# Kernel optimization log

Measured on AMD Instinct MI355X. Metric: run time of the kernel, lower is better.

The kernel has to match this reference:

```python
import jax, jax.numpy as jnp
import numpy as np

HARDSHRINK_LAMBDA = 0.75

def setup_inputs() -> dict:
    key = jax.random.key(0)
    k1, k2, k3, k4, k5 = jax.random.split(key, 5)
    B, Cin, H, W = 32, 3, 128, 128
    Cmid, Dout = 256, 4096
    x = jax.random.normal(k1, (B, Cin, H, W), dtype=jnp.float32)
    # Conv2d(3,256,k=3,p=1) params, kaiming-ish scale
    conv_w = jax.random.normal(k2, (Cmid, Cin, 3, 3), dtype=jnp.float32) * (1.0 / np.sqrt(Cin * 9))
    conv_b = jax.random.normal(k3, (Cmid,), dtype=jnp.float32) * 0.01
    fc_w = jax.random.normal(k4, (Dout, Cmid), dtype=jnp.float32) * (1.0 / np.sqrt(Cmid))
    fc_b = jax.random.normal(k5, (Dout,), dtype=jnp.float32) * 0.01
    return {"x": x, "conv_w": conv_w, "conv_b": conv_b, "fc_w": fc_w, "fc_b": fc_b}

def reference(x, conv_w, conv_b, fc_w, fc_b):
    # Conv2d stride=1, padding=1  -> [B, Cmid, H, W]
    y = jax.lax.conv_general_dilated(
        x, conv_w, window_strides=(1, 1), padding=((1, 1), (1, 1)),
        dimension_numbers=("NCHW", "OIHW", "NCHW"))
    y = y + conv_b[None, :, None, None]
    y = jax.nn.relu(y)
    # Nearest upsample (integer scale) replicates each value s*s times; the
    # subsequent elementwise hardshrink then global average pool is therefore
    y = jnp.where(jnp.abs(y) > HARDSHRINK_LAMBDA, y, 0.0)
    pooled = jnp.mean(y, axis=(2, 3))  # [B, Cmid]
    out = pooled @ fc_w.T + fc_b       # [B, Dout]
    return jax.nn.log_sigmoid(out)
```

## Files before the change

kernel.cpp:

```cpp
#include <hip/hip_runtime.h>
#include <hip/hip_bf16.h>

#define LAMBDA 0.75f
#define CMID 256
#define DOUT 4096

typedef __attribute__((ext_vector_type(8))) short bf16x8;
typedef __attribute__((ext_vector_type(4))) float f32x4;

static inline __device__ short f2bf(float f) {
    __hip_bfloat16 h = __float2bfloat16(f);
    short s; __builtin_memcpy(&s, &h, 2);
    return s;
}
static inline __device__ unsigned pack2(float lo, float hi) {
    unsigned a = (unsigned short)f2bf(lo);
    unsigned b = (unsigned short)f2bf(hi);
    return a | (b << 16);
}

__global__ __launch_bounds__(256, 2) void conv_pool_mfma(
    const float* __restrict__ x, const float* __restrict__ conv_w,
    const float* __restrict__ conv_b, float* __restrict__ pooled)
{
    __shared__ float    raw[3 * 4 * 136];
    __shared__ unsigned im2col[256 * 20];

    const int b  = blockIdx.x >> 6;
    const int h0 = (blockIdx.x & 63) * 2;
    const int t  = threadIdx.x;
    const int l  = t & 63;
    const int wv = t >> 6;
    const int lm = l & 15;
    const int g  = l >> 4;

    for (int i = t; i < 1632; i += 256) {
        int ci  = i / 544;
        int rem = i - ci * 544;
        int r   = rem / 136;
        int idx = rem - r * 136;
        int hh  = h0 - 1 + r;
        int col = idx - 4;
        float v = 0.f;
        if ((unsigned)hh < 128u && (unsigned)col < 128u)
            v = x[(b * 3 + ci) * 16384 + hh * 128 + col];
        raw[i] = v;
    }

    bf16x8 wfrag[4];
    f32x4  biasf[4], pool[4];
    #pragma unroll
    for (int c = 0; c < 4; ++c) {
        const int ct = wv * 4 + c;
        const int co = ct * 16 + lm;
        const float* wp = conv_w + co * 27;
        float av[8];
        if (g < 3) {
            #pragma unroll
            for (int j = 0; j < 8; ++j) av[j] = wp[g * 9 + j];
        } else {
            av[0] = wp[8]; av[1] = wp[17]; av[2] = wp[26];
            av[3] = av[4] = av[5] = av[6] = av[7] = 0.f;
        }
        #pragma unroll
        for (int j = 0; j < 8; ++j) wfrag[c][j] = f2bf(av[j]);
        const float bb = conv_b[co];
        biasf[c] = (f32x4){bb, bb, bb, bb};
        pool[c]  = (f32x4){0.f, 0.f, 0.f, 0.f};
    }

    __syncthreads();

    {
        const int out_r = t >> 7;
        const int px    = t & 127;
        unsigned* dst = &im2col[t * 20];
        const float* r0 = raw + 0 * 544 + out_r * 136 + px + 3;
        const float* r1 = raw + 1 * 544 + out_r * 136 + px + 3;
        const float* r2 = raw + 2 * 544 + out_r * 136 + px + 3;
        uint4 w;
        w.x = pack2(r0[0],   r0[1]);   w.y = pack2(r0[2],   r0[136]);
        w.z = pack2(r0[137], r0[138]); w.w = pack2(r0[272], r0[273]);
        *(uint4*)(dst + 0) = w;
        w.x = pack2(r1[0],   r1[1]);   w.y = pack2(r1[2],   r1[136]);
        w.z = pack2(r1[137], r1[138]); w.w = pack2(r1[272], r1[273]);
        *(uint4*)(dst + 4) = w;
        w.x = pack2(r2[0],   r2[1]);   w.y = pack2(r2[2],   r2[136]);
        w.z = pack2(r2[137], r2[138]); w.w = pack2(r2[272], r2[273]);
        *(uint4*)(dst + 8) = w;
        w.x = pack2(r0[274], r1[274]); w.y = pack2(r2[274], 0.f);
        w.z = 0u;                      w.w = 0u;
        *(uint4*)(dst + 12) = w;
    }

    __syncthreads();

    #pragma unroll
    for (int tile = 0; tile < 16; ++tile) {
        const uint4 xr = *(const uint4*)&im2col[(tile * 16 + lm) * 20 + g * 4];
        bf16x8 xf; __builtin_memcpy(&xf, &xr, 16);
        #pragma unroll
        for (int c = 0; c < 4; ++c) {
            f32x4 acc = __builtin_amdgcn_mfma_f32_16x16x32_bf16(
                xf, wfrag[c], biasf[c], 0, 0, 0);
            #pragma unroll
            for (int r = 0; r < 4; ++r)
                pool[c][r] += (acc[r] > LAMBDA) ? acc[r] : 0.f;
        }
    }

    #pragma unroll
    for (int c = 0; c < 4; ++c) {
        float s = (pool[c][0] + pool[c][1]) + (pool[c][2] + pool[c][3]);
        s += __shfl_xor(s, 16, 64);
        s += __shfl_xor(s, 32, 64);
        if (l < 16)
            atomicAdd(&pooled[b * CMID + (wv * 4 + c) * 16 + lm], s);
    }
}

__global__ __launch_bounds__(256) void fc_kernel(
    const float* __restrict__ pooled, const float* __restrict__ fc_w,
    const float* __restrict__ fc_b, float* __restrict__ out)
{
    __shared__ float pool[CMID];
    const int b = blockIdx.y;
    const int t = threadIdx.x;
    pool[t] = pooled[b * CMID + t] * (1.0f / 16384.0f);
    __syncthreads();

    const int d = blockIdx.x * 256 + t;
    const float4* wrow = (const float4*)(fc_w + d * CMID);
    float acc = fc_b[d];
    #pragma unroll 8
    for (int k4 = 0; k4 < CMID / 4; k4++) {
        float4 wv = wrow[k4];
        acc += wv.x * pool[k4 * 4 + 0] + wv.y * pool[k4 * 4 + 1]
             + wv.z * pool[k4 * 4 + 2] + wv.w * pool[k4 * 4 + 3];
    }
    float ls = fminf(acc, 0.f) - log1pf(expf(-fabsf(acc)));
    out[b * (int)DOUT + d] = ls;
}

extern "C" void kernel_launch(void* const* d_in, const int* in_sizes, int n_in,
                              void* d_out, int out_size, void* d_ws, size_t ws_size,
                              hipStream_t stream) {
    const float* x      = (const float*)d_in[0];
    const float* conv_w = (const float*)d_in[1];
    const float* conv_b = (const float*)d_in[2];
    const float* fc_w   = (const float*)d_in[3];
    const float* fc_b   = (const float*)d_in[4];
    float* out = (float*)d_out;

    float* pooled = (float*)d_ws;

    hipMemsetAsync(pooled, 0, 32 * CMID * sizeof(float), stream);
    conv_pool_mfma<<<32 * 64, 256, 0, stream>>>(x, conv_w, conv_b, pooled);
    fc_kernel<<<dim3(16, 32), 256, 0, stream>>>(pooled, fc_w, fc_b, out);
}
```

Measured before the change: 51.72 us.

## Replace atomic pooling with per-block partials and transpose im2col LDS layout

The conv kernel now writes per-block partial channel sums to a workspace buffer instead of atomically adding into a pooled buffer. The fc kernel reduces the 64 partials per batch itself, which removes the memset launch and the global atomics. The im2col shared buffer is reorganised into four planes of uint4 indexed by thread, so both the writes and the MFMA-operand reads are contiguous and avoid bank conflicts from the old stride-20 layout. The cost is a larger workspace and 64 extra strided loads per thread in each fc block, repeated across its 16 column blocks.

```diff
diff --git a/kernel.cpp b/kernel.cpp
--- a/kernel.cpp
+++ b/kernel.cpp
@@ -21,13 +21,14 @@
 
 __global__ __launch_bounds__(256, 2) void conv_pool_mfma(
     const float* __restrict__ x, const float* __restrict__ conv_w,
-    const float* __restrict__ conv_b, float* __restrict__ pooled)
+    const float* __restrict__ conv_b, float* __restrict__ part)
 {
-    __shared__ float    raw[3 * 4 * 136];
-    __shared__ unsigned im2col[256 * 20];
+    __shared__ float raw[1632];
+    __shared__ uint4 im2col[4][256];
 
-    const int b  = blockIdx.x >> 6;
-    const int h0 = (blockIdx.x & 63) * 2;
+    const int bk = blockIdx.x;
+    const int b  = bk >> 6;
+    const int h0 = (bk & 63) * 2;
     const int t  = threadIdx.x;
     const int l  = t & 63;
     const int wv = t >> 6;
@@ -74,30 +75,29 @@
     {
         const int out_r = t >> 7;
         const int px    = t & 127;
-        unsigned* dst = &im2col[t * 20];
         const float* r0 = raw + 0 * 544 + out_r * 136 + px + 3;
         const float* r1 = raw + 1 * 544 + out_r * 136 + px + 3;
         const float* r2 = raw + 2 * 544 + out_r * 136 + px + 3;
         uint4 w;
         w.x = pack2(r0[0],   r0[1]);   w.y = pack2(r0[2],   r0[136]);
         w.z = pack2(r0[137], r0[138]); w.w = pack2(r0[272], r0[273]);
-        *(uint4*)(dst + 0) = w;
+        im2col[0][t] = w;
         w.x = pack2(r1[0],   r1[1]);   w.y = pack2(r1[2],   r1[136]);
         w.z = pack2(r1[137], r1[138]); w.w = pack2(r1[272], r1[273]);
-        *(uint4*)(dst + 4) = w;
+        im2col[1][t] = w;
         w.x = pack2(r2[0],   r2[1]);   w.y = pack2(r2[2],   r2[136]);
         w.z = pack2(r2[137], r2[138]); w.w = pack2(r2[272], r2[273]);
-        *(uint4*)(dst + 8) = w;
+        im2col[2][t] = w;
         w.x = pack2(r0[274], r1[274]); w.y = pack2(r2[274], 0.f);
         w.z = 0u;                      w.w = 0u;
-        *(uint4*)(dst + 12) = w;
+        im2col[3][t] = w;
     }
 
     __syncthreads();
 
     #pragma unroll
     for (int tile = 0; tile < 16; ++tile) {
-        const uint4 xr = *(const uint4*)&im2col[(tile * 16 + lm) * 20 + g * 4];
+        const uint4 xr = im2col[g][tile * 16 + lm];
         bf16x8 xf; __builtin_memcpy(&xf, &xr, 16);
         #pragma unroll
         for (int c = 0; c < 4; ++c) {
@@ -115,18 +115,23 @@
         s += __shfl_xor(s, 16, 64);
         s += __shfl_xor(s, 32, 64);
         if (l < 16)
-            atomicAdd(&pooled[b * CMID + (wv * 4 + c) * 16 + lm], s);
+            part[bk * 256 + wv * 64 + c * 16 + lm] = s;
     }
 }
 
 __global__ __launch_bounds__(256) void fc_kernel(
-    const float* __restrict__ pooled, const float* __restrict__ fc_w,
+    const float* __restrict__ part, const float* __restrict__ fc_w,
     const float* __restrict__ fc_b, float* __restrict__ out)
 {
     __shared__ float pool[CMID];
     const int b = blockIdx.y;
     const int t = threadIdx.x;
-    pool[t] = pooled[b * CMID + t] * (1.0f / 16384.0f);
+
+    float s = 0.f;
+    const float* pp = part + b * 64 * 256 + t;
+    #pragma unroll
+    for (int j = 0; j < 64; ++j) s += pp[j * 256];
+    pool[t] = s * (1.0f / 16384.0f);
     __syncthreads();
 
     const int d = blockIdx.x * 256 + t;
@@ -152,9 +157,8 @@
     const float* fc_b   = (const float*)d_in[4];
     float* out = (float*)d_out;
 
-    float* pooled = (float*)d_ws;
+    float* part = (float*)d_ws;
 
-    hipMemsetAsync(pooled, 0, 32 * CMID * sizeof(float), stream);
-    conv_pool_mfma<<<32 * 64, 256, 0, stream>>>(x, conv_w, conv_b, pooled);
-    fc_kernel<<<dim3(16, 32), 256, 0, stream>>>(pooled, fc_w, fc_b, out);
+    conv_pool_mfma<<<32 * 64, 256, 0, stream>>>(x, conv_w, conv_b, part);
+    fc_kernel<<<dim3(16, 32), 256, 0, stream>>>(part, fc_w, fc_b, out);
 }
```

New measurement: 51.66 us. No clear change (-0.1%).
